# Performance work log

Hardware: AMD Instinct MI355X
Metric: run time of the kernel (lower is better)

The kernel has to match this reference:

```python
import jax, jax.numpy as jnp
import numpy as np

N_NODES = 100000
N_EDGES = 1600000
F_IN = 128
F_HID = 128
BN_EPS = 1e-5


def setup_inputs() -> dict:
    key = jax.random.key(0)
    ks = jax.random.split(key, 8)
    x = jax.random.normal(ks[0], (N_NODES, F_IN), dtype=jnp.float32)
    edge_row = jax.random.randint(ks[1], (N_EDGES,), 0, N_NODES, dtype=jnp.int32)
    edge_col = jax.random.randint(ks[2], (N_EDGES,), 0, N_NODES, dtype=jnp.int32)
    edge_weight = jax.random.uniform(ks[3], (N_EDGES,), dtype=jnp.float32)
    # Glorot-ish init for the two GCN layer weights
    W1 = jax.random.normal(ks[4], (F_IN, F_HID), dtype=jnp.float32) * (1.0 / np.sqrt(F_IN))
    b1 = jnp.zeros((F_HID,), dtype=jnp.float32)
    W2 = jax.random.normal(ks[5], (F_HID, F_HID), dtype=jnp.float32) * (1.0 / np.sqrt(F_HID))
    b2 = jnp.zeros((F_HID,), dtype=jnp.float32)
    gamma = jnp.ones((F_HID,), dtype=jnp.float32)
    beta = jnp.zeros((F_HID,), dtype=jnp.float32)
    return {"x": x, "edge_row": edge_row, "edge_col": edge_col,
            "edge_weight": edge_weight, "W1": W1, "b1": b1,
            "W2": W2, "b2": b2, "gamma": gamma, "beta": beta}


def _spmm(row, col, w, dense):
    # sparse [N,N] @ dense [N,F] via gather + segment_sum (COO)
    gathered = dense[col] * w[:, None]           # [E, F]
    return jax.ops.segment_sum(gathered, row, num_segments=N_NODES)


def _batchnorm(h, gamma, beta):
    # BatchNorm1d in training mode: batch statistics over node dim
    mean = jnp.mean(h, axis=0)
    var = jnp.var(h, axis=0)
    return gamma * (h - mean) * jax.lax.rsqrt(var + BN_EPS) + beta


def reference(x, edge_row, edge_col, edge_weight, W1, b1, W2, b2, gamma, beta):
    # Layer 1: GCN conv = adj @ (x @ W1) + b1
    h = _spmm(edge_row, edge_col, edge_weight, x @ W1) + b1
    # BN -> ReLU (dropout is identity in deterministic/eval reference)
    h = jax.nn.relu(_batchnorm(h, gamma, beta))
    # Layer 2: GCN conv
    out = _spmm(edge_row, edge_col, edge_weight, h @ W2) + b2
    return out
```

## Files before the change

### kernel.cpp

```cpp
#include <hip/hip_runtime.h>

#define F    128
#define FQ   32
#define FU   64
#define RPB  128
#define BSH  7
#define TILE 2048
#define SCAP 4096
#define LSTR 68

typedef __attribute__((ext_vector_type(8))) short short8;
typedef __attribute__((ext_vector_type(4))) float f32x4;

__device__ __forceinline__ unsigned int f2bf2(float a, float b) {
    unsigned int ua = __float_as_uint(a);
    unsigned int ub = __float_as_uint(b);
    ua = (ua + 0x7fffu + ((ua >> 16) & 1u)) >> 16;
    ub = (ub + 0x7fffu + ((ub >> 16) & 1u)) >> 16;
    return ua | (ub << 16);
}
__device__ __forceinline__ unsigned short f2bf1(float a) {
    unsigned int ua = __float_as_uint(a);
    return (unsigned short)((ua + 0x7fffu + ((ua >> 16) & 1u)) >> 16);
}

template <bool BN>
__global__ __launch_bounds__(256) void gemm_kernel(const float* __restrict__ X,
                                                   const float* __restrict__ W,
                                                   const float* __restrict__ ac,
                                                   unsigned int* __restrict__ Hb,
                                                   int nNodes) {
    __shared__ unsigned int XtU[64 * LSTR];
    __shared__ unsigned int WtU[128 * LSTR];

    const int tid = threadIdx.x;
    const int bn0 = blockIdx.x * 64;

    {
        int f = tid >> 1;
        int kh = (tid & 1) * 64;
        #pragma unroll
        for (int k8 = 0; k8 < 8; ++k8) {
            int k0 = kh + k8 * 8;
            float v[8];
            #pragma unroll
            for (int i = 0; i < 8; ++i) v[i] = W[(size_t)(k0 + i) * F + f];
            uint4 pk;
            pk.x = f2bf2(v[0], v[1]);
            pk.y = f2bf2(v[2], v[3]);
            pk.z = f2bf2(v[4], v[5]);
            pk.w = f2bf2(v[6], v[7]);
            *(uint4*)&WtU[f * LSTR + k0 / 2] = pk;
        }
    }
    {
        const float4* X4 = (const float4*)X;
        const float4* A4 = (const float4*)ac;
        const float4* C4 = (const float4*)(ac + F);
        #pragma unroll
        for (int it = 0; it < 8; ++it) {
            int i = tid + it * 256;
            int n = i >> 5;
            int kq = i & 31;
            int node = bn0 + n;
            float4 v = make_float4(0.f, 0.f, 0.f, 0.f);
            if (node < nNodes) v = X4[(size_t)node * FQ + kq];
            if (BN) {
                float4 a = A4[kq], c = C4[kq];
                v.x = fmaxf(fmaf(a.x, v.x, c.x), 0.f);
                v.y = fmaxf(fmaf(a.y, v.y, c.y), 0.f);
                v.z = fmaxf(fmaf(a.z, v.z, c.z), 0.f);
                v.w = fmaxf(fmaf(a.w, v.w, c.w), 0.f);
            }
            uint2 pk = make_uint2(f2bf2(v.x, v.y), f2bf2(v.z, v.w));
            *(uint2*)&XtU[n * LSTR + kq * 2] = pk;
        }
    }
    __syncthreads();

    const int l = tid & 63;
    const int wv = tid >> 6;
    const int quad = l >> 4, lo = l & 15;
    const int fb = wv * 32;

    f32x4 acc[4][2];
    #pragma unroll
    for (int nt = 0; nt < 4; ++nt)
        #pragma unroll
        for (int ft = 0; ft < 2; ++ft) acc[nt][ft] = (f32x4){0.f, 0.f, 0.f, 0.f};

    #pragma unroll
    for (int kc = 0; kc < 4; ++kc) {
        int koff = kc * 16 + quad * 4;
        short8 a[4], b[2];
        #pragma unroll
        for (int nt = 0; nt < 4; ++nt)
            a[nt] = *(const short8*)&XtU[(nt * 16 + lo) * LSTR + koff];
        #pragma unroll
        for (int ft = 0; ft < 2; ++ft)
            b[ft] = *(const short8*)&WtU[(fb + ft * 16 + lo) * LSTR + koff];
        #pragma unroll
        for (int nt = 0; nt < 4; ++nt)
            #pragma unroll
            for (int ft = 0; ft < 2; ++ft)
                acc[nt][ft] = __builtin_amdgcn_mfma_f32_16x16x32_bf16(
                    a[nt], b[ft], acc[nt][ft], 0, 0, 0);
    }

    unsigned short* Hs = (unsigned short*)Hb;
    #pragma unroll
    for (int nt = 0; nt < 4; ++nt) {
        #pragma unroll
        for (int reg = 0; reg < 4; ++reg) {
            int node = bn0 + nt * 16 + quad * 4 + reg;
            if (node < nNodes) {
                #pragma unroll
                for (int ft = 0; ft < 2; ++ft)
                    Hs[(size_t)node * F + fb + ft * 16 + lo] = f2bf1(acc[nt][ft][reg]);
            }
        }
    }
}

__global__ __launch_bounds__(256) void histo_kernel(const int* __restrict__ row,
                                                    int* __restrict__ hist,
                                                    int NB, int E) {
    __shared__ int h[1024];
    int t = threadIdx.x;
    for (int i = t; i < NB; i += 256) h[i] = 0;
    __syncthreads();
    int base = blockIdx.x * TILE + t * 8;
    if (base + 7 < E) {
        int4 a = ((const int4*)row)[(base >> 2) + 0];
        int4 b = ((const int4*)row)[(base >> 2) + 1];
        atomicAdd(&h[a.x >> BSH], 1); atomicAdd(&h[a.y >> BSH], 1);
        atomicAdd(&h[a.z >> BSH], 1); atomicAdd(&h[a.w >> BSH], 1);
        atomicAdd(&h[b.x >> BSH], 1); atomicAdd(&h[b.y >> BSH], 1);
        atomicAdd(&h[b.z >> BSH], 1); atomicAdd(&h[b.w >> BSH], 1);
    } else {
        for (int j = 0; j < 8; ++j)
            if (base + j < E) atomicAdd(&h[row[base + j] >> BSH], 1);
    }
    __syncthreads();
    for (int i = t; i < NB; i += 256) hist[(size_t)blockIdx.x * NB + i] = h[i];
}

__global__ __launch_bounds__(256) void btot_kernel(const int* __restrict__ hist,
                                                   int* __restrict__ total,
                                                   int nT, int NB) {
    int b = blockIdx.x;
    int s = 0;
    for (int t = threadIdx.x; t < nT; t += 256) s += hist[(size_t)t * NB + b];
    __shared__ int red[256];
    red[threadIdx.x] = s;
    __syncthreads();
    for (int o = 128; o > 0; o >>= 1) {
        if (threadIdx.x < o) red[threadIdx.x] += red[threadIdx.x + o];
        __syncthreads();
    }
    if (threadIdx.x == 0) total[b] = red[0];
}

__global__ __launch_bounds__(1024) void bstart_kernel(const int* __restrict__ total,
                                                      int* __restrict__ start,
                                                      int NB, int E) {
    __shared__ int sh[1024];
    int t = threadIdx.x;
    int v = (t < NB) ? total[t] : 0;
    sh[t] = v;
    __syncthreads();
    #pragma unroll
    for (int o = 1; o < 1024; o <<= 1) {
        int add = (t >= o) ? sh[t - o] : 0;
        __syncthreads();
        sh[t] += add;
        __syncthreads();
    }
    if (t < NB) start[t] = sh[t] - v;
    if (t == 0) start[NB] = E;
}

__global__ __launch_bounds__(1024) void boff_kernel(const int* __restrict__ hist,
                                                    const int* __restrict__ start,
                                                    int* __restrict__ off,
                                                    int nT, int NB) {
    __shared__ int sh[1024];
    int b = blockIdx.x, t = threadIdx.x;
    int v = (t < nT) ? hist[(size_t)t * NB + b] : 0;
    sh[t] = v;
    __syncthreads();
    #pragma unroll
    for (int o = 1; o < 1024; o <<= 1) {
        int add = (t >= o) ? sh[t - o] : 0;
        __syncthreads();
        sh[t] += add;
        __syncthreads();
    }
    if (t < nT) off[(size_t)b * nT + t] = start[b] + sh[t] - v;
}

__global__ __launch_bounds__(256) void bplace_kernel(const int* __restrict__ row,
                                                     const int* __restrict__ col,
                                                     const float* __restrict__ w,
                                                     const int* __restrict__ off,
                                                     int2* __restrict__ tmp,
                                                     int nT, int NB, int E) {
    __shared__ int h[1024];
    int t = threadIdx.x, tile = blockIdx.x;
    for (int i = t; i < NB; i += 256) h[i] = 0;
    __syncthreads();
    int base = tile * TILE + t * 8;
    int r[8], c[8];
    float ww[8];
    int nv = 0;
    if (base + 7 < E) {
        int4 ra = ((const int4*)row)[(base >> 2) + 0];
        int4 rb = ((const int4*)row)[(base >> 2) + 1];
        int4 ca = ((const int4*)col)[(base >> 2) + 0];
        int4 cb = ((const int4*)col)[(base >> 2) + 1];
        float4 wa = ((const float4*)w)[(base >> 2) + 0];
        float4 wb = ((const float4*)w)[(base >> 2) + 1];
        r[0] = ra.x; r[1] = ra.y; r[2] = ra.z; r[3] = ra.w;
        r[4] = rb.x; r[5] = rb.y; r[6] = rb.z; r[7] = rb.w;
        c[0] = ca.x; c[1] = ca.y; c[2] = ca.z; c[3] = ca.w;
        c[4] = cb.x; c[5] = cb.y; c[6] = cb.z; c[7] = cb.w;
        ww[0] = wa.x; ww[1] = wa.y; ww[2] = wa.z; ww[3] = wa.w;
        ww[4] = wb.x; ww[5] = wb.y; ww[6] = wb.z; ww[7] = wb.w;
        nv = 8;
    } else {
        for (int j = 0; j < 8; ++j)
            if (base + j < E) { r[nv] = row[base + j]; c[nv] = col[base + j];
                                ww[nv] = w[base + j]; ++nv; }
    }
    #pragma unroll 8
    for (int j = 0; j < 8; ++j) {
        if (j >= nv) break;
        int b = r[j] >> BSH;
        int rank = atomicAdd(&h[b], 1);
        int pos = off[(size_t)b * nT + tile] + rank;
        tmp[pos] = make_int2(((r[j] & (RPB - 1)) << 25) | c[j], __float_as_int(ww[j]));
    }
}

__global__ __launch_bounds__(256) void bsort_kernel(const int2* __restrict__ tmp,
                                                    const int* __restrict__ start,
                                                    int2* __restrict__ pairs,
                                                    int* __restrict__ rowptr,
                                                    int N, int NB, int E) {
    __shared__ int cntB[RPB];
    __shared__ int cntS[RPB];
    __shared__ int sc[RPB];
    __shared__ int2 outP[SCAP];
    int b = blockIdx.x, t = threadIdx.x;
    int s0 = start[b], s1 = start[b + 1];
    int len = s1 - s0;
    if (len > SCAP) len = SCAP;

    if (t < RPB) cntB[t] = 0;
    __syncthreads();

    int2 p[16];
    int np = 0;
    #pragma unroll
    for (int k = 0; k < 16; ++k) {
        int i = t + k * 256;
        if (i < len) { p[k] = tmp[s0 + i]; ++np; }
    }
    #pragma unroll
    for (int k = 0; k < 16; ++k) {
        if (k >= np) break;
        atomicAdd(&cntB[((unsigned)p[k].x) >> 25], 1);
    }
    __syncthreads();
    int val = (t < RPB) ? cntB[t] : 0;
    if (t < RPB) sc[t] = val;
    __syncthreads();
    #pragma unroll
    for (int o = 1; o < RPB; o <<= 1) {
        int add = (t < RPB && t >= o) ? sc[t - o] : 0;
        __syncthreads();
        if (t < RPB) sc[t] += add;
        __syncthreads();
    }
    if (t < RPB) { int ex = sc[t] - val; cntB[t] = ex; cntS[t] = ex; }
    __syncthreads();
    #pragma unroll
    for (int k = 0; k < 16; ++k) {
        if (k >= np) break;
        int rl = ((unsigned)p[k].x) >> 25;
        int lr = atomicAdd(&cntB[rl], 1);
        outP[lr] = make_int2(p[k].x & 0x1ffffff, p[k].y);
    }
    __syncthreads();
    for (int i = t; i < len; i += 256) pairs[s0 + i] = outP[i];
    int r0 = b * RPB;
    if (t < RPB && r0 + t < N) rowptr[r0 + t] = s0 + cntS[t];
    if (b == NB - 1 && t == 0) rowptr[N] = E;
}

__global__ __launch_bounds__(256) void spmm_csr_kernel(const int* __restrict__ rowptr,
                                                       const int2* __restrict__ pairs,
                                                       const unsigned int* __restrict__ Hb,
                                                       const float* __restrict__ bias,
                                                       float* __restrict__ out, int N) {
    int r = blockIdx.x * 4 + (threadIdx.x >> 6);
    if (r >= N) return;
    int l = threadIdx.x & 63;
    float2 acc = bias ? ((const float2*)bias)[l] : make_float2(0.f, 0.f);
    int i = rowptr[r], end = rowptr[r + 1];

    for (; i + 16 <= end; i += 16) {
        int2 p[16];
        #pragma unroll
        for (int j = 0; j < 16; ++j) p[j] = pairs[i + j];
        unsigned int g[16];
        #pragma unroll
        for (int j = 0; j < 16; ++j) g[j] = Hb[(size_t)p[j].x * FU + l];
        #pragma unroll
        for (int j = 0; j < 16; ++j) {
            float wt = __int_as_float(p[j].y);
            acc.x = fmaf(wt, __uint_as_float(g[j] << 16), acc.x);
            acc.y = fmaf(wt, __uint_as_float(g[j] & 0xffff0000u), acc.y);
        }
    }
    if (i + 8 <= end) {
        int2 p[8];
        #pragma unroll
        for (int j = 0; j < 8; ++j) p[j] = pairs[i + j];
        unsigned int g[8];
        #pragma unroll
        for (int j = 0; j < 8; ++j) g[j] = Hb[(size_t)p[j].x * FU + l];
        #pragma unroll
        for (int j = 0; j < 8; ++j) {
            float wt = __int_as_float(p[j].y);
            acc.x = fmaf(wt, __uint_as_float(g[j] << 16), acc.x);
            acc.y = fmaf(wt, __uint_as_float(g[j] & 0xffff0000u), acc.y);
        }
        i += 8;
    }
    if (i + 4 <= end) {
        int2 p[4];
        #pragma unroll
        for (int j = 0; j < 4; ++j) p[j] = pairs[i + j];
        unsigned int g[4];
        #pragma unroll
        for (int j = 0; j < 4; ++j) g[j] = Hb[(size_t)p[j].x * FU + l];
        #pragma unroll
        for (int j = 0; j < 4; ++j) {
            float wt = __int_as_float(p[j].y);
            acc.x = fmaf(wt, __uint_as_float(g[j] << 16), acc.x);
            acc.y = fmaf(wt, __uint_as_float(g[j] & 0xffff0000u), acc.y);
        }
        i += 4;
    }
    for (; i < end; ++i) {
        int2 p = pairs[i];
        unsigned int g = Hb[(size_t)p.x * FU + l];
        float wt = __int_as_float(p.y);
        acc.x = fmaf(wt, __uint_as_float(g << 16), acc.x);
        acc.y = fmaf(wt, __uint_as_float(g & 0xffff0000u), acc.y);
    }
    ((float2*)out)[(size_t)r * 64 + l] = acc;
}

__global__ __launch_bounds__(256) void bnstats_kernel(const float* __restrict__ H,
                                                      float* __restrict__ sums,
                                                      int nNodes) {
    int f = threadIdx.x & 127;
    int g = threadIdx.x >> 7;
    int stride = gridDim.x * 2;
    float s = 0.f, sq = 0.f;
    for (int n = blockIdx.x * 2 + g; n < nNodes; n += stride) {
        float v = H[(size_t)n * F + f];
        s += v;
        sq = fmaf(v, v, sq);
    }
    __shared__ float red[256];
    red[threadIdx.x] = s;
    __syncthreads();
    float sfull = 0.f;
    if (g == 0) sfull = red[f] + red[f + 128];
    __syncthreads();
    red[threadIdx.x] = sq;
    __syncthreads();
    if (g == 0) {
        float sqfull = red[f] + red[f + 128];
        atomicAdd(&sums[f], sfull);
        atomicAdd(&sums[128 + f], sqfull);
    }
}

__global__ void bnfinal_kernel(const float* __restrict__ sums,
                               const float* __restrict__ gamma,
                               const float* __restrict__ beta,
                               float* __restrict__ ac, float invN) {
    int f = threadIdx.x;
    float mean = sums[f] * invN;
    float var = sums[128 + f] * invN - mean * mean;
    float a = gamma[f] * rsqrtf(var + 1e-5f);
    ac[f] = a;
    ac[128 + f] = beta[f] - mean * a;
}

extern "C" void kernel_launch(void* const* d_in, const int* in_sizes, int n_in,
                              void* d_out, int out_size, void* d_ws, size_t ws_size,
                              hipStream_t stream) {
    const float* x    = (const float*)d_in[0];
    const int*   erow = (const int*)d_in[1];
    const int*   ecol = (const int*)d_in[2];
    const float* ew   = (const float*)d_in[3];
    const float* W1   = (const float*)d_in[4];
    const float* W2   = (const float*)d_in[6];
    const float* b2   = (const float*)d_in[7];
    const float* gmm  = (const float*)d_in[8];
    const float* beta = (const float*)d_in[9];
    float* out = (float*)d_out;

    const int N = in_sizes[0] / F;
    const int E = in_sizes[1];

    const int NB = (N + RPB - 1) / RPB;
    const int nT = (E + TILE - 1) / TILE;

    float*        buf1   = (float*)d_ws;
    unsigned int* Hb     = (unsigned int*)(buf1 + (size_t)N * F);
    float*        stats  = (float*)(Hb + (size_t)N * FU);
    float*        ac     = stats + 256;
    int*          rowptr = (int*)(ac + 256);
    int*          start  = rowptr + N + 2;
    int*          total  = start + 1028;
    int*          hist   = total + 1024;
    int*          off    = hist + (size_t)nT * NB;
    int2*         tmp    = (int2*)(off + (size_t)NB * nT);
    int2*         pairs  = tmp + E;

    const int gemmGrid = (N + 63) / 64;
    const int spmmGrid = (N + 3) / 4;

    hipMemsetAsync(stats, 0, 256 * sizeof(float), stream);

    histo_kernel<<<nT, 256, 0, stream>>>(erow, hist, NB, E);
    btot_kernel<<<NB, 256, 0, stream>>>(hist, total, nT, NB);
    bstart_kernel<<<1, 1024, 0, stream>>>(total, start, NB, E);
    boff_kernel<<<NB, 1024, 0, stream>>>(hist, start, off, nT, NB);
    bplace_kernel<<<nT, 256, 0, stream>>>(erow, ecol, ew, off, tmp, nT, NB, E);
    bsort_kernel<<<NB, 256, 0, stream>>>(tmp, start, pairs, rowptr, N, NB, E);

    gemm_kernel<false><<<gemmGrid, 256, 0, stream>>>(x, W1, nullptr, Hb, N);
    spmm_csr_kernel<<<spmmGrid, 256, 0, stream>>>(rowptr, pairs, Hb, nullptr, buf1, N);
    bnstats_kernel<<<400, 256, 0, stream>>>(buf1, stats, N);
    bnfinal_kernel<<<1, 128, 0, stream>>>(stats, gmm, beta, ac, 1.0f / (float)N);
    gemm_kernel<true><<<gemmGrid, 256, 0, stream>>>(buf1, W2, ac, Hb, N);
    spmm_csr_kernel<<<spmmGrid, 256, 0, stream>>>(rowptr, pairs, Hb, b2, out, N);
}
```

Measured before the change: 416.7 us.

## Store layer-1 SpMM output as bf16 and gather 16-byte rows per quarter-wave

The first SpMM now writes its intermediate result in bf16 instead of fp32, and the BN-stats and second GEMM kernels read that packed format. This halves the traffic for the intermediate buffer. The SpMM kernel is also restructured so each quarter-wave handles a different edge with 16-byte vector gathers, followed by a cross-quarter shuffle reduction. In exchange, the intermediate is rounded to bf16 before the batchnorm statistics are taken, and shuffle overhead is added on top of a padded tail edge.

Measured after the change: 398.5 us. -4.4%, faster.

```diff
diff --git a/kernel.cpp b/kernel.cpp
--- a/kernel.cpp
+++ b/kernel.cpp
@@ -25,7 +25,7 @@
 }
 
 template <bool BN>
-__global__ __launch_bounds__(256) void gemm_kernel(const float* __restrict__ X,
+__global__ __launch_bounds__(256) void gemm_kernel(const void* __restrict__ Xv,
                                                    const float* __restrict__ W,
                                                    const float* __restrict__ ac,
                                                    unsigned int* __restrict__ Hb,
@@ -54,7 +54,6 @@
         }
     }
     {
-        const float4* X4 = (const float4*)X;
         const float4* A4 = (const float4*)ac;
         const float4* C4 = (const float4*)(ac + F);
         #pragma unroll
@@ -63,16 +62,26 @@
             int n = i >> 5;
             int kq = i & 31;
             int node = bn0 + n;
-            float4 v = make_float4(0.f, 0.f, 0.f, 0.f);
-            if (node < nNodes) v = X4[(size_t)node * FQ + kq];
+            uint2 pk = make_uint2(0u, 0u);
             if (BN) {
+                uint2 raw = make_uint2(0u, 0u);
+                if (node < nNodes) raw = ((const uint2*)Xv)[(size_t)node * 32 + kq];
+                float4 v;
+                v.x = __uint_as_float(raw.x << 16);
+                v.y = __uint_as_float(raw.x & 0xffff0000u);
+                v.z = __uint_as_float(raw.y << 16);
+                v.w = __uint_as_float(raw.y & 0xffff0000u);
                 float4 a = A4[kq], c = C4[kq];
                 v.x = fmaxf(fmaf(a.x, v.x, c.x), 0.f);
                 v.y = fmaxf(fmaf(a.y, v.y, c.y), 0.f);
                 v.z = fmaxf(fmaf(a.z, v.z, c.z), 0.f);
                 v.w = fmaxf(fmaf(a.w, v.w, c.w), 0.f);
+                pk = make_uint2(f2bf2(v.x, v.y), f2bf2(v.z, v.w));
+            } else {
+                float4 v = make_float4(0.f, 0.f, 0.f, 0.f);
+                if (node < nNodes) v = ((const float4*)Xv)[(size_t)node * FQ + kq];
+                pk = make_uint2(f2bf2(v.x, v.y), f2bf2(v.z, v.w));
             }
-            uint2 pk = make_uint2(f2bf2(v.x, v.y), f2bf2(v.z, v.w));
             *(uint2*)&XtU[n * LSTR + kq * 2] = pk;
         }
     }
@@ -298,95 +307,117 @@
     if (b == NB - 1 && t == 0) rowptr[N] = E;
 }
 
+template <bool BF16OUT>
 __global__ __launch_bounds__(256) void spmm_csr_kernel(const int* __restrict__ rowptr,
                                                        const int2* __restrict__ pairs,
                                                        const unsigned int* __restrict__ Hb,
                                                        const float* __restrict__ bias,
-                                                       float* __restrict__ out, int N) {
+                                                       void* __restrict__ outv, int N) {
     int r = blockIdx.x * 4 + (threadIdx.x >> 6);
     if (r >= N) return;
-    int l = threadIdx.x & 63;
-    float2 acc = bias ? ((const float2*)bias)[l] : make_float2(0.f, 0.f);
+    const int l = threadIdx.x & 63;
+    const int g = l >> 4, q = l & 15;
+    const uint4* H4 = (const uint4*)Hb;
+
+    float acc[8];
+    #pragma unroll
+    for (int j = 0; j < 8; ++j) acc[j] = 0.f;
+
     int i = rowptr[r], end = rowptr[r + 1];
 
     for (; i + 16 <= end; i += 16) {
-        int2 p[16];
-        #pragma unroll
-        for (int j = 0; j < 16; ++j) p[j] = pairs[i + j];
-        unsigned int g[16];
-        #pragma unroll
-        for (int j = 0; j < 16; ++j) g[j] = Hb[(size_t)p[j].x * FU + l];
-        #pragma unroll
-        for (int j = 0; j < 16; ++j) {
-            float wt = __int_as_float(p[j].y);
-            acc.x = fmaf(wt, __uint_as_float(g[j] << 16), acc.x);
-            acc.y = fmaf(wt, __uint_as_float(g[j] & 0xffff0000u), acc.y);
-        }
-    }
-    if (i + 8 <= end) {
-        int2 p[8];
-        #pragma unroll
-        for (int j = 0; j < 8; ++j) p[j] = pairs[i + j];
-        unsigned int g[8];
-        #pragma unroll
-        for (int j = 0; j < 8; ++j) g[j] = Hb[(size_t)p[j].x * FU + l];
-        #pragma unroll
-        for (int j = 0; j < 8; ++j) {
-            float wt = __int_as_float(p[j].y);
-            acc.x = fmaf(wt, __uint_as_float(g[j] << 16), acc.x);
-            acc.y = fmaf(wt, __uint_as_float(g[j] & 0xffff0000u), acc.y);
-        }
-        i += 8;
-    }
-    if (i + 4 <= end) {
         int2 p[4];
-        #pragma unroll
-        for (int j = 0; j < 4; ++j) p[j] = pairs[i + j];
-        unsigned int g[4];
-        #pragma unroll
-        for (int j = 0; j < 4; ++j) g[j] = Hb[(size_t)p[j].x * FU + l];
+        uint4 gv[4];
+        #pragma unroll
+        for (int k = 0; k < 4; ++k) p[k] = pairs[i + 4 * k + g];
+        #pragma unroll
+        for (int k = 0; k < 4; ++k) gv[k] = H4[(size_t)p[k].x * 16 + q];
+        #pragma unroll
+        for (int k = 0; k < 4; ++k) {
+            float wt = __int_as_float(p[k].y);
+            unsigned int uu[4] = {gv[k].x, gv[k].y, gv[k].z, gv[k].w};
+            #pragma unroll
+            for (int j = 0; j < 4; ++j) {
+                acc[2 * j]     = fmaf(wt, __uint_as_float(uu[j] << 16), acc[2 * j]);
+                acc[2 * j + 1] = fmaf(wt, __uint_as_float(uu[j] & 0xffff0000u), acc[2 * j + 1]);
+            }
+        }
+    }
+    for (; i + 4 <= end; i += 4) {
+        int2 p = pairs[i + g];
+        uint4 gv = H4[(size_t)p.x * 16 + q];
+        float wt = __int_as_float(p.y);
+        unsigned int uu[4] = {gv.x, gv.y, gv.z, gv.w};
         #pragma unroll
         for (int j = 0; j < 4; ++j) {
-            float wt = __int_as_float(p[j].y);
-            acc.x = fmaf(wt, __uint_as_float(g[j] << 16), acc.x);
-            acc.y = fmaf(wt, __uint_as_float(g[j] & 0xffff0000u), acc.y);
-        }
-        i += 4;
-    }
-    for (; i < end; ++i) {
-        int2 p = pairs[i];
-        unsigned int g = Hb[(size_t)p.x * FU + l];
+            acc[2 * j]     = fmaf(wt, __uint_as_float(uu[j] << 16), acc[2 * j]);
+            acc[2 * j + 1] = fmaf(wt, __uint_as_float(uu[j] & 0xffff0000u), acc[2 * j + 1]);
+        }
+    }
+    if (i < end) {
+        int e = i + g;
+        int2 p = (e < end) ? pairs[e] : make_int2(0, 0);
+        uint4 gv = H4[(size_t)p.x * 16 + q];
         float wt = __int_as_float(p.y);
-        acc.x = fmaf(wt, __uint_as_float(g << 16), acc.x);
-        acc.y = fmaf(wt, __uint_as_float(g & 0xffff0000u), acc.y);
-    }
-    ((float2*)out)[(size_t)r * 64 + l] = acc;
-}
-
-__global__ __launch_bounds__(256) void bnstats_kernel(const float* __restrict__ H,
+        unsigned int uu[4] = {gv.x, gv.y, gv.z, gv.w};
+        #pragma unroll
+        for (int j = 0; j < 4; ++j) {
+            acc[2 * j]     = fmaf(wt, __uint_as_float(uu[j] << 16), acc[2 * j]);
+            acc[2 * j + 1] = fmaf(wt, __uint_as_float(uu[j] & 0xffff0000u), acc[2 * j + 1]);
+        }
+    }
+
+    #pragma unroll
+    for (int j = 0; j < 8; ++j) {
+        acc[j] += __shfl_xor(acc[j], 16, 64);
+        acc[j] += __shfl_xor(acc[j], 32, 64);
+    }
+
+    if (g == 0) {
+        if (bias) {
+            float4 b0 = ((const float4*)bias)[q * 2];
+            float4 b1 = ((const float4*)bias)[q * 2 + 1];
+            acc[0] += b0.x; acc[1] += b0.y; acc[2] += b0.z; acc[3] += b0.w;
+            acc[4] += b1.x; acc[5] += b1.y; acc[6] += b1.z; acc[7] += b1.w;
+        }
+        if (BF16OUT) {
+            uint4 pk;
+            pk.x = f2bf2(acc[0], acc[1]);
+            pk.y = f2bf2(acc[2], acc[3]);
+            pk.z = f2bf2(acc[4], acc[5]);
+            pk.w = f2bf2(acc[6], acc[7]);
+            ((uint4*)outv)[(size_t)r * 16 + q] = pk;
+        } else {
+            float4* o = (float4*)outv;
+            o[(size_t)r * 32 + q * 2]     = make_float4(acc[0], acc[1], acc[2], acc[3]);
+            o[(size_t)r * 32 + q * 2 + 1] = make_float4(acc[4], acc[5], acc[6], acc[7]);
+        }
+    }
+}
+
+__global__ __launch_bounds__(256) void bnstats_kernel(const unsigned int* __restrict__ Hu,
                                                       float* __restrict__ sums,
                                                       int nNodes) {
-    int f = threadIdx.x & 127;
-    int g = threadIdx.x >> 7;
-    int stride = gridDim.x * 2;
-    float s = 0.f, sq = 0.f;
-    for (int n = blockIdx.x * 2 + g; n < nNodes; n += stride) {
-        float v = H[(size_t)n * F + f];
-        s += v;
-        sq = fmaf(v, v, sq);
-    }
-    __shared__ float red[256];
-    red[threadIdx.x] = s;
-    __syncthreads();
-    float sfull = 0.f;
-    if (g == 0) sfull = red[f] + red[f + 128];
-    __syncthreads();
-    red[threadIdx.x] = sq;
+    int u = threadIdx.x & 63;
+    int g = threadIdx.x >> 6;
+    int stride = gridDim.x * 4;
+    float s0 = 0.f, s1 = 0.f, q0 = 0.f, q1 = 0.f;
+    for (int n = blockIdx.x * 4 + g; n < nNodes; n += stride) {
+        unsigned int v = Hu[(size_t)n * FU + u];
+        float a = __uint_as_float(v << 16);
+        float b = __uint_as_float(v & 0xffff0000u);
+        s0 += a; s1 += b;
+        q0 = fmaf(a, a, q0); q1 = fmaf(b, b, q1);
+    }
+    __shared__ float4 red[256];
+    red[threadIdx.x] = make_float4(s0, s1, q0, q1);
     __syncthreads();
     if (g == 0) {
-        float sqfull = red[f] + red[f + 128];
-        atomicAdd(&sums[f], sfull);
-        atomicAdd(&sums[128 + f], sqfull);
+        float4 r0 = red[u], r1 = red[64 + u], r2 = red[128 + u], r3 = red[192 + u];
+        atomicAdd(&sums[2 * u],       r0.x + r1.x + r2.x + r3.x);
+        atomicAdd(&sums[2 * u + 1],   r0.y + r1.y + r2.y + r3.y);
+        atomicAdd(&sums[128 + 2 * u],     r0.z + r1.z + r2.z + r3.z);
+        atomicAdd(&sums[128 + 2 * u + 1], r0.w + r1.w + r2.w + r3.w);
     }
 }
 
@@ -422,8 +453,8 @@
     const int NB = (N + RPB - 1) / RPB;
     const int nT = (E + TILE - 1) / TILE;
 
-    float*        buf1   = (float*)d_ws;
-    unsigned int* Hb     = (unsigned int*)(buf1 + (size_t)N * F);
+    unsigned int* buf1   = (unsigned int*)d_ws;
+    unsigned int* Hb     = buf1 + (size_t)N * FU;
     float*        stats  = (float*)(Hb + (size_t)N * FU);
     float*        ac     = stats + 256;
     int*          rowptr = (int*)(ac + 256);
@@ -447,9 +478,11 @@
     bsort_kernel<<<NB, 256, 0, stream>>>(tmp, start, pairs, rowptr, N, NB, E);
 
     gemm_kernel<false><<<gemmGrid, 256, 0, stream>>>(x, W1, nullptr, Hb, N);
-    spmm_csr_kernel<<<spmmGrid, 256, 0, stream>>>(rowptr, pairs, Hb, nullptr, buf1, N);
+    spmm_csr_kernel<true><<<spmmGrid, 256, 0, stream>>>(rowptr, pairs, Hb,
+                                                        nullptr, buf1, N);
     bnstats_kernel<<<400, 256, 0, stream>>>(buf1, stats, N);
     bnfinal_kernel<<<1, 128, 0, stream>>>(stats, gmm, beta, ac, 1.0f / (float)N);
     gemm_kernel<true><<<gemmGrid, 256, 0, stream>>>(buf1, W2, ac, Hb, N);
-    spmm_csr_kernel<<<spmmGrid, 256, 0, stream>>>(rowptr, pairs, Hb, b2, out, N);
-}
+    spmm_csr_kernel<false><<<spmmGrid, 256, 0, stream>>>(rowptr, pairs, Hb,
+                                                         b2, out, N);
+}
```
